# Kernel tuning notes

Hardware: AMD Instinct MI355X
Metric: run time of the kernel (lower is better)

Reference implementation:

```python
import jax, jax.numpy as jnp
import numpy as np

B = 262144
D = 128          # d_model
DFF = 4 * D      # 512, FFN expansion
T = 16           # num_tiles
TPC = 4          # tiles_per_cluster
NC = T // TPC    # 4 clusters
NOPS = 8         # len(OPCODES)
EMB = 32
FEAT = EMB + 17  # 49
TW, SW, DW = 0.01, 0.005, 0.01  # ternary / sparsity / diversity weights


def ternary_quant(W):
    # per-tile ternary quantization: threshold at 0.7 * mean|W|, scale = mean|W|
    s0 = jnp.mean(jnp.abs(W))
    return s0 * jnp.sign(W) * (jnp.abs(W) > 0.7 * s0).astype(W.dtype)


def setup_inputs() -> dict:
    key = jax.random.key(0)
    ks = jax.random.split(key, 16)
    inp = {
        'op_idx': jax.random.randint(ks[0], (B,), 0, NOPS),
        'a': jax.random.randint(ks[1], (B,), 0, 256),
        'b': jax.random.randint(ks[2], (B,), 0, 256),
        'c': jax.random.randint(ks[3], (B,), 0, 2),
        # parameters
        'op_embed': jax.random.normal(ks[4], (NOPS, EMB), jnp.float32),
        'W_in': jax.random.normal(ks[5], (FEAT, D), jnp.float32) / np.sqrt(FEAT),
        'b_in': jnp.zeros((D,), jnp.float32),
        'Wr': jax.random.normal(ks[6], (D, T), jnp.float32) / np.sqrt(D),
        'W1': jax.random.normal(ks[7], (T, D, DFF), jnp.float32) / np.sqrt(D),
        'W2': jax.random.normal(ks[8], (T, DFF, D), jnp.float32) / np.sqrt(DFF),
        'Wh1': jax.random.normal(ks[9], (D, 64), jnp.float32) / np.sqrt(D),
        'bh1': jnp.zeros((64,), jnp.float32),
        'Wh2': jax.random.normal(ks[10], (64, 8), jnp.float32) / np.sqrt(64),
        'bh2': jnp.zeros((8,), jnp.float32),
    }
    return inp


def reference(op_embed, W_in, b_in, Wr, W1, W2, Wh1, bh1, Wh2, bh2, op_idx, a, b, c):
    bits = lambda v: ((v[:, None] >> jnp.arange(8)) & 1).astype(jnp.float32)  # [B,8]
    emb = op_embed[op_idx]  # [B,32]
    x = jnp.concatenate([emb, bits(a), bits(b), c[:, None].astype(jnp.float32)], axis=1)  # [B,49]
    x = x @ W_in + b_in  # [B,D]

    # tile routing (top-1)
    logits = x @ Wr                      # [B,T]
    probs = jax.nn.softmax(logits, -1)
    idx = jnp.argmax(probs, -1)          # [B]
    gate = jnp.max(probs, -1)            # [B]

    # ternary-quantized per-tile FFN weights
    W1q = jax.vmap(ternary_quant)(W1)    # [T,D,DFF]
    W2q = jax.vmap(ternary_quant)(W2)    # [T,DFF,D]

    out = jnp.zeros_like(x)
    for t in range(T):  # fixed small tile set
        y = jax.nn.gelu(x @ W1q[t]) @ W2q[t]          # [B,D]
        out = out + jnp.where((idx == t)[:, None], y, 0.0)
    out = out * gate[:, None]

    # aux losses
    one_hot = jax.nn.one_hot(idx, T, dtype=x.dtype)
    frac = one_hot.mean(0)               # tokens per tile
    meanp = probs.mean(0)                # mean router prob per tile
    sparsity = T * jnp.sum(frac * meanp)              # load-balance (Switch-style)
    tern = jnp.mean(jnp.abs(W1 - W1q)) + jnp.mean(jnp.abs(W2 - W2q))
    cp = meanp.reshape(NC, TPC).sum(-1)               # cluster usage
    diversity = jnp.sum(cp * jnp.log(cp + 1e-9))      # negative entropy
    aux = TW * tern + SW * sparsity + DW * diversity

    h = jax.nn.relu(out @ Wh1 + bh1)
    result = jax.nn.sigmoid(h @ Wh2 + bh2)  # [B,8]
    return result, idx, aux
```

## Files before the change

### kernel.cpp

```cpp
#include <hip/hip_runtime.h>
#include <hip/hip_bf16.h>
#include <math.h>

typedef __attribute__((ext_vector_type(8))) short short8;
typedef __attribute__((ext_vector_type(4))) float floatx4;
typedef __attribute__((ext_vector_type(4))) unsigned int uintx4;

#define BUCKET_CAP 262144

__device__ __forceinline__ unsigned short f2bf(float f) {
    unsigned int u = __float_as_uint(f);
    unsigned int r = (u + 0x7fffu + ((u >> 16) & 1u)) >> 16;
    return (unsigned short)r;
}

__device__ __forceinline__ unsigned int cvtpk(float a, float b) {
    unsigned int r;
    asm("v_cvt_pk_bf16_f32 %0, %1, %2" : "=v"(r) : "v"(a), "v"(b));
    return r;
}

__device__ __forceinline__ void permlane32_swap(unsigned int &a, unsigned int &b) {
    asm volatile("v_permlane32_swap_b32 %0, %1" : "+v"(a), "+v"(b));
}
__device__ __forceinline__ void permlane16_swap(unsigned int &a, unsigned int &b) {
    asm volatile("v_permlane16_swap_b32 %0, %1" : "+v"(a), "+v"(b));
}

__device__ __forceinline__ float gelu_f(float u) {
    float u2 = u * u;
    float p = __builtin_fmaf(u2, -0.102943242f, -2.302208184f);
    float z = p * u;
    float e;
    asm("v_exp_f32 %0, %1" : "=v"(e) : "v"(z));
    return u * __builtin_amdgcn_rcpf(1.0f + e);
}

__device__ __forceinline__ floatx4 mfma16(short8 a, short8 b, floatx4 c) {
    return __builtin_amdgcn_mfma_f32_16x16x32_bf16(a, b, c, 0, 0, 0);
}


__global__ __launch_bounds__(256) void k_prep1(
        const float* __restrict__ W1, const float* __restrict__ W2,
        float* __restrict__ partials,
        const float* __restrict__ op_embed, const float* __restrict__ W_in,
        const float* __restrict__ b_in,
        float* embW, float* Ta, float* Tb, float* Tc,
        int* __restrict__ accz) {
    __shared__ float red[256];
    int bid = blockIdx.x;
    if (bid < 512) {
        bool isW1 = bid < 256;
        const float* W = (isW1 ? W1 : W2) + (long)(isW1 ? bid : bid - 256) * 4096;
        float s = 0.f;
        #pragma unroll
        for (int i = 0; i < 4; i++) {
            floatx4 v = *(const floatx4*)(W + i * 1024 + threadIdx.x * 4);
            s += fabsf(v[0]) + fabsf(v[1]) + fabsf(v[2]) + fabsf(v[3]);
        }
        red[threadIdx.x] = s; __syncthreads();
        for (int st = 128; st > 0; st >>= 1) {
            if (threadIdx.x < st) red[threadIdx.x] += red[threadIdx.x + st];
            __syncthreads();
        }
        if (threadIdx.x == 0) partials[bid] = red[0];
    } else {
        int i = (bid - 512) * 256 + threadIdx.x;
        if (i < 1024) {
            int op = i >> 7, j = i & 127;
            float s = b_in[j];
            #pragma unroll
            for (int k = 0; k < 32; k++) s += op_embed[op * 32 + k] * W_in[k * 128 + j];
            embW[i] = s;
        } else if (i < 1024 + 32768) {
            int r = i - 1024; int a = r >> 7, j = r & 127;
            float s = 0.f;
            #pragma unroll
            for (int bit = 0; bit < 8; bit++) if ((a >> bit) & 1) s += W_in[(32 + bit) * 128 + j];
            Ta[r] = s;
        } else if (i < 33792 + 32768) {
            int r = i - 33792; int b = r >> 7, j = r & 127;
            float s = 0.f;
            #pragma unroll
            for (int bit = 0; bit < 8; bit++) if ((b >> bit) & 1) s += W_in[(40 + bit) * 128 + j];
            Tb[r] = s;
        } else if (i < 66560 + 128) {
            int j = i - 66560; Tc[j] = W_in[48 * 128 + j];
        } else if (i < 66688 + 64) {
            accz[i - 66688] = 0;
        }
    }
}


__global__ __launch_bounds__(256) void k_prep2(
        const float* __restrict__ W1, const float* __restrict__ W2,
        const float* __restrict__ partials,
        unsigned short* __restrict__ W1qT, unsigned short* __restrict__ W2qT,
        float* ternsum,
        const float* __restrict__ embW, const float* __restrict__ Ta,
        const float* __restrict__ Tb, const float* __restrict__ Tc,
        const float* __restrict__ Wr,
        float* embWr, float* TaR, float* TbR, float* TcR) {
    __shared__ unsigned short Lq[4096];
    __shared__ float red[256];
    int blk = blockIdx.x;
    if (blk >= 512) {
        int i = (blk - 512) * 256 + threadIdx.x;
        int row = i >> 4, t = i & 15;
        const float* src; float* dst;
        if (row < 8)        { src = embW + row * 128;        dst = embWr + i; }
        else if (row < 264) { src = Ta + (row - 8) * 128;    dst = TaR + (row - 8) * 16 + t; }
        else if (row < 520) { src = Tb + (row - 264) * 128;  dst = TbR + (row - 264) * 16 + t; }
        else if (row == 520){ src = Tc;                      dst = TcR + t; }
        else return;
        float s = 0.f;
        for (int j = 0; j < 128; j++) s += src[j] * Wr[j * 16 + t];
        *dst = s;
        return;
    }
    bool isW1 = blk < 256;
    int rb = isW1 ? blk : blk - 256;
    int t = rb >> 4, slab = rb & 15;
    const float* part = partials + (isW1 ? 0 : 256) + t * 16;
    float ssum = 0.f;
    #pragma unroll
    for (int i = 0; i < 16; i++) ssum += part[i];
    float s = ssum * (1.0f / 65536.0f);
    float thr = 0.7f * s;
    unsigned int us = (unsigned int)f2bf(s);
    int tid = threadIdx.x;
    float dsum = 0.f;
    if (isW1) {
        int f0 = slab * 32;
        int d = tid >> 1, fh = (tid & 1) * 16;
        const float* src = W1 + (long)t * 65536 + d * 512 + f0 + fh;
        #pragma unroll
        for (int i = 0; i < 4; i++) {
            floatx4 w = *(const floatx4*)(src + i * 4);
            #pragma unroll
            for (int r = 0; r < 4; r++) {
                float wv = w[r];
                float aw = fabsf(wv);
                bool big = aw > thr;
                dsum += big ? fabsf(aw - s) : aw;
                unsigned int sign15 = (__float_as_uint(wv) >> 16) & 0x8000u;
                unsigned short q = big ? (unsigned short)(us | sign15) : (unsigned short)0;
                Lq[(fh + i * 4 + r) * 128 + d] = q;
            }
        }
    } else {
        int d0 = slab * 8;
        int f = tid * 2;
        const float* src = W2 + (long)t * 65536 + f * 128 + d0;
        #pragma unroll
        for (int rr = 0; rr < 2; rr++) {
            #pragma unroll
            for (int i = 0; i < 2; i++) {
                floatx4 w = *(const floatx4*)(src + rr * 128 + i * 4);
                #pragma unroll
                for (int r = 0; r < 4; r++) {
                    float wv = w[r];
                    float aw = fabsf(wv);
                    bool big = aw > thr;
                    dsum += big ? fabsf(aw - s) : aw;
                    unsigned int sign15 = (__float_as_uint(wv) >> 16) & 0x8000u;
                    unsigned short q = big ? (unsigned short)(us | sign15) : (unsigned short)0;
                    Lq[(i * 4 + r) * 512 + f + rr] = q;
                }
            }
        }
    }
    __syncthreads();
    unsigned short* dst = (isW1 ? W1qT : W2qT) + (long)t * 65536 + slab * 4096;
    const uintx4* Ls = (const uintx4*)Lq;
    uintx4* D4 = (uintx4*)dst;
    D4[tid] = Ls[tid];
    D4[tid + 256] = Ls[tid + 256];
    red[tid] = dsum; __syncthreads();
    for (int st2 = 128; st2 > 0; st2 >>= 1) {
        if (tid < st2) red[tid] += red[tid + st2];
        __syncthreads();
    }
    if (tid == 0) atomicAdd(ternsum, red[0]);
}


__global__ __launch_bounds__(256) void k_main3(
        const int* __restrict__ op_idx, const int* __restrict__ a_in,
        const int* __restrict__ b_in_i, const int* __restrict__ c_in,
        const float* __restrict__ embWr, const float* __restrict__ TaR,
        const float* __restrict__ TbR, const float* __restrict__ TcR,
        float2* __restrict__ rec_out,
        float* psum, int* cnt, int* fill, int* __restrict__ bucket,
        float* __restrict__ d_idx,
        const unsigned short* __restrict__ W2qT, const float* __restrict__ Wh1,
        unsigned short* __restrict__ W23qT) {
    __shared__ float sp[4][16];
    __shared__ int sc[4][16];
    __shared__ float wcol[128];
    __shared__ int lc[16], lbase[16];
    __shared__ unsigned char blE[256];
    __shared__ unsigned char lpE[256];

    if (blockIdx.x >= 1024) {
        int b2 = blockIdx.x - 1024;
        int t = b2 >> 6, h = b2 & 63;
        if (threadIdx.x < 128) wcol[threadIdx.x] = Wh1[threadIdx.x * 64 + h];
        __syncthreads();
        int k2 = threadIdx.x * 2;
        const unsigned short* w2 = W2qT + (long)t * 65536 + k2;
        float a0 = 0.f, a1 = 0.f;
        #pragma unroll 8
        for (int d = 0; d < 128; d++) {
            unsigned int u = *(const unsigned int*)(w2 + d * 512);
            float w = wcol[d];
            a0 += w * __uint_as_float(u << 16);
            a1 += w * __uint_as_float(u & 0xffff0000u);
        }
        *(unsigned int*)(W23qT + ((long)(t * 64 + h)) * 512 + k2) = cvtpk(a0, a1);
        return;
    }

    int tid = threadIdx.x;
    if (tid < 16) lc[tid] = 0;
    __syncthreads();

    int lane = tid & 63;
    int j = lane & 15;
    int grpbase = lane & 48;
    int tl = tid >> 4;
    float psum_acc = 0.f; int cnt_acc = 0;

    #pragma unroll 1
    for (int it = 0; it < 16; it++) {
        int tok = blockIdx.x * 256 + it * 16 + tl;
        int op = op_idx[tok], a = a_in[tok], b = b_in_i[tok], c = c_in[tok];
        float cf = (float)c;

        float lg = embWr[op * 16 + j] + TaR[a * 16 + j] + TbR[b * 16 + j] + cf * TcR[j];
        float m = lg;
        m = fmaxf(m, __shfl_xor(m, 8, 16));
        m = fmaxf(m, __shfl_xor(m, 4, 16));
        m = fmaxf(m, __shfl_xor(m, 2, 16));
        m = fmaxf(m, __shfl_xor(m, 1, 16));
        float p = __expf(lg - m);
        float s = p;
        s += __shfl_xor(s, 8, 16);
        s += __shfl_xor(s, 4, 16);
        s += __shfl_xor(s, 2, 16);
        s += __shfl_xor(s, 1, 16);
        float g = __builtin_amdgcn_rcpf(s);
        unsigned long long ball = __ballot(lg == m);
        int bi = __ffsll((unsigned long long)((ball >> grpbase) & 0xffffULL)) - 1;
        psum_acc += p * g;
        cnt_acc += (j == bi) ? 1 : 0;
        if (j == bi) {
            int lpos = atomicAdd(&lc[bi], 1);
            int e = it * 16 + tl;
            blE[e] = (unsigned char)bi;
            lpE[e] = (unsigned char)lpos;
        }
        if (j == 0) {
            unsigned int desc = (unsigned int)op | ((unsigned int)a << 3)
                              | ((unsigned int)b << 11) | ((unsigned int)c << 19);
            float2 rr; rr.x = __uint_as_float(desc); rr.y = g;
            rec_out[tok] = rr;
            d_idx[tok] = (float)bi;
        }
    }

    psum_acc += __shfl_xor(psum_acc, 16);
    psum_acc += __shfl_xor(psum_acc, 32);
    cnt_acc += __shfl_xor(cnt_acc, 16);
    cnt_acc += __shfl_xor(cnt_acc, 32);
    int wv = tid >> 6;
    if (lane < 16) { sp[wv][j] = psum_acc; sc[wv][j] = cnt_acc; }
    __syncthreads();
    if (tid < 16) {
        atomicAdd(&psum[tid], sp[0][tid] + sp[1][tid] + sp[2][tid] + sp[3][tid]);
        atomicAdd(&cnt[tid], sc[0][tid] + sc[1][tid] + sc[2][tid] + sc[3][tid]);
        lbase[tid] = atomicAdd(&fill[tid], lc[tid]);
    }
    __syncthreads();
    {
        int e = tid;
        int bi = (int)blE[e];
        int tok = blockIdx.x * 256 + e;
        bucket[bi * BUCKET_CAP + lbase[bi] + (int)lpE[e]] = tok;
    }
}


__global__ __launch_bounds__(256, 3) void k_ffn(
    const float2* __restrict__ rec,
    const float* __restrict__ embW, const float* __restrict__ Ta,
    const float* __restrict__ Tb, const float* __restrict__ Tc,
    const int* __restrict__ bucket, const int* __restrict__ cnt_g,
    const float* __restrict__ psum_g, const float* __restrict__ ternsum_g,
    const unsigned short* __restrict__ W1qT, const unsigned short* __restrict__ W23qT,
    const float* __restrict__ Wh2, const float* __restrict__ bh1,
    const float* __restrict__ bh2,
    float* __restrict__ result, float* __restrict__ d_aux) {

    extern __shared__ __align__(16) unsigned char smem[];
    unsigned short* Ax = (unsigned short*)smem;
    float* Red = (float*)(smem + 17408);
    int*   toks = (int*)(smem + 33792);
    float* gats = (float*)(smem + 34048);
    float* Wh2l = (float*)(smem + 34304);
    float* bh2l = (float*)(smem + 36352);
    float* bh1l = (float*)(smem + 36384);
    int*   opsl = (int*)(smem + 36640);
    int*   asl  = (int*)(smem + 36896);
    int*   bsl  = (int*)(smem + 37152);
    float* csl  = (float*)(smem + 37408);
    int*   cntl = (int*)(smem + 37664);

    int bid = blockIdx.x;
    int tid = threadIdx.x;

    if (tid < 16) cntl[tid] = cnt_g[tid];
    __syncthreads();
    int t = -1, ci = 0, nt = 0, base = 0;
    {
        int coff = 0;
        #pragma unroll
        for (int tt = 0; tt < 16; tt++) {
            int c = cntl[tt];
            int ch = (c + 63) >> 6;
            if (t < 0 && bid < coff + ch) {
                t = tt; ci = bid - coff; nt = c;
                base = tt * BUCKET_CAP + ci * 64;
            }
            coff += ch;
        }
    }
    if (t < 0) return;
    int nvalid = nt - ci * 64; if (nvalid > 64) nvalid = 64;

    if (tid < 64) {
        int tk = (tid < nvalid) ? bucket[base + tid] : -1;
        toks[tid] = tk;
        int tks = (tk >= 0) ? tk : 0;
        float2 rd = rec[tks];
        unsigned int desc = __float_as_uint(rd.x);
        gats[tid] = (tk >= 0) ? rd.y : 0.0f;
        opsl[tid] = (int)(desc & 7u);
        asl[tid]  = (int)((desc >> 3) & 255u);
        bsl[tid]  = (int)((desc >> 11) & 255u);
        csl[tid]  = (float)((desc >> 19) & 1u);
    }
    Wh2l[tid] = Wh2[tid];
    Wh2l[tid + 256] = Wh2[tid + 256];
    if (tid < 8) bh2l[tid] = bh2[tid];
    else if (tid < 72) bh1l[tid - 8] = bh1[tid - 8];
    __syncthreads();

    #pragma unroll
    for (int it = 0; it < 4; it++) {
        int seg = it * 256 + tid; int r = seg >> 4, sg = seg & 15;
        int d0 = sg * 8;
        int op = opsl[r], a = asl[r], b = bsl[r];
        float cf = csl[r];
        const floatx4* Ev = (const floatx4*)(embW + op * 128 + d0);
        const floatx4* A4 = (const floatx4*)(Ta + a * 128 + d0);
        const floatx4* B4 = (const floatx4*)(Tb + b * 128 + d0);
        const floatx4* C4 = (const floatx4*)(Tc + d0);
        floatx4 v0 = Ev[0] + A4[0] + B4[0] + cf * C4[0];
        floatx4 v1 = Ev[1] + A4[1] + B4[1] + cf * C4[1];
        uintx4 o;
        o[0] = cvtpk(v0[0], v0[1]);
        o[1] = cvtpk(v0[2], v0[3]);
        o[2] = cvtpk(v1[0], v1[1]);
        o[3] = cvtpk(v1[2], v1[3]);
        *(uintx4*)(Ax + r * 136 + sg * 8) = o;
    }
    __syncthreads();

    int lane = tid & 63, dh = tid >> 6;
    int lane15 = lane & 15, lgrp = lane >> 4;

    floatx4 acc3[4][4];
    #pragma unroll
    for (int i = 0; i < 4; i++)
        #pragma unroll
        for (int j = 0; j < 4; j++) acc3[i][j] = (floatx4){0.f, 0.f, 0.f, 0.f};

    const unsigned short* w1p  = W1qT + (long)t * 65536 + (dh * 32 + lane15) * 128 + lgrp * 8;
    const unsigned short* w23p = W23qT + (long)t * 32768 + lane15 * 512 + dh * 32 + lgrp * 8;
    int ho0 = dh * 8192;
    int ho1 = ((dh + 1) & 3) * 8192;
    int ho2 = ((dh + 2) & 3) * 8192;
    int ho3 = ((dh + 3) & 3) * 8192;

    #pragma unroll
    for (int nc = 0; nc < 4; nc++) {
        const unsigned short* w1c = w1p + nc * 16384;
        const unsigned short* w23c = w23p + nc * 128;

        short8 a00 = *(const short8*)(w1c + 0 * 32);
        short8 a01 = *(const short8*)(w1c + 1 * 32);
        short8 a02 = *(const short8*)(w1c + 2 * 32);
        short8 a03 = *(const short8*)(w1c + 3 * 32);
        short8 a10 = *(const short8*)(w1c + 2048 + 0 * 32);
        short8 a11 = *(const short8*)(w1c + 2048 + 1 * 32);
        short8 a12 = *(const short8*)(w1c + 2048 + 2 * 32);
        short8 a13 = *(const short8*)(w1c + 2048 + 3 * 32);
        short8 af23_0 = *(const short8*)(w23c + ho0);
        short8 af23_1 = *(const short8*)(w23c + ho1);
        short8 af23_2 = *(const short8*)(w23c + ho2);
        short8 af23_3 = *(const short8*)(w23c + ho3);

        floatx4 acc1[2][4];
        #pragma unroll
        for (int i = 0; i < 2; i++)
            #pragma unroll
            for (int j = 0; j < 4; j++) acc1[i][j] = (floatx4){0.f, 0.f, 0.f, 0.f};

        #pragma unroll
        for (int mt = 0; mt < 4; mt++) {
            int mrow = (mt * 16 + lane15) * 136;
            short8 bf0 = *(const short8*)(Ax + mrow + 0 * 32 + lgrp * 8);
            short8 bf1 = *(const short8*)(Ax + mrow + 1 * 32 + lgrp * 8);
            short8 bf2 = *(const short8*)(Ax + mrow + 2 * 32 + lgrp * 8);
            short8 bf3 = *(const short8*)(Ax + mrow + 3 * 32 + lgrp * 8);
            acc1[0][mt] = mfma16(a00, bf0, acc1[0][mt]);
            acc1[1][mt] = mfma16(a10, bf0, acc1[1][mt]);
            acc1[0][mt] = mfma16(a01, bf1, acc1[0][mt]);
            acc1[1][mt] = mfma16(a11, bf1, acc1[1][mt]);
            acc1[0][mt] = mfma16(a02, bf2, acc1[0][mt]);
            acc1[1][mt] = mfma16(a12, bf2, acc1[1][mt]);
            acc1[0][mt] = mfma16(a03, bf3, acc1[0][mt]);
            acc1[1][mt] = mfma16(a13, bf3, acc1[1][mt]);
        }

        #pragma unroll
        for (int mt = 0; mt < 4; mt++) {
            floatx4 v0 = acc1[0][mt], v1 = acc1[1][mt];
            unsigned int X0 = cvtpk(gelu_f(v0[0]), gelu_f(v0[1]));
            unsigned int X1 = cvtpk(gelu_f(v0[2]), gelu_f(v0[3]));
            unsigned int Y0 = cvtpk(gelu_f(v1[0]), gelu_f(v1[1]));
            unsigned int Y1 = cvtpk(gelu_f(v1[2]), gelu_f(v1[3]));
            permlane32_swap(X0, Y0);
            permlane16_swap(X0, Y0);
            permlane32_swap(X1, Y1);
            permlane16_swap(X1, Y1);
            union { uintx4 u; short8 s; } bu;
            bu.u[0] = X0; bu.u[1] = X1; bu.u[2] = Y0; bu.u[3] = Y1;
            short8 bfrag = bu.s;
            acc3[0][mt] = mfma16(af23_0, bfrag, acc3[0][mt]);
            acc3[1][mt] = mfma16(af23_1, bfrag, acc3[1][mt]);
            acc3[2][mt] = mfma16(af23_2, bfrag, acc3[2][mt]);
            acc3[3][mt] = mfma16(af23_3, bfrag, acc3[3][mt]);
        }
    }

    floatx4 fin[4];
    #pragma unroll
    for (int mt = 0; mt < 4; mt++) fin[mt] = acc3[0][mt];
    float* myslot = Red + dh * 1024;
    int lofs = lane * 4;
    #pragma unroll
    for (int mt = 0; mt < 4; mt++)
        *(floatx4*)(myslot + mt * 256 + lofs) = acc3[1][mt];
    __syncthreads();
    {
        const float* ps = Red + ((dh + 3) & 3) * 1024;
        #pragma unroll
        for (int mt = 0; mt < 4; mt++)
            fin[mt] += *(const floatx4*)(ps + mt * 256 + lofs);
    }
    __syncthreads();
    #pragma unroll
    for (int mt = 0; mt < 4; mt++)
        *(floatx4*)(myslot + mt * 256 + lofs) = acc3[2][mt];
    __syncthreads();
    {
        const float* ps = Red + ((dh + 2) & 3) * 1024;
        #pragma unroll
        for (int mt = 0; mt < 4; mt++)
            fin[mt] += *(const floatx4*)(ps + mt * 256 + lofs);
    }
    __syncthreads();
    #pragma unroll
    for (int mt = 0; mt < 4; mt++)
        *(floatx4*)(myslot + mt * 256 + lofs) = acc3[3][mt];
    __syncthreads();
    {
        const float* ps = Red + ((dh + 1) & 3) * 1024;
        #pragma unroll
        for (int mt = 0; mt < 4; mt++)
            fin[mt] += *(const floatx4*)(ps + mt * 256 + lofs);
    }

    float* H = (float*)Ax;
    int hb = dh * 16 + lgrp * 4;
    floatx4 b4 = *(const floatx4*)(bh1l + hb);
    #pragma unroll
    for (int mt = 0; mt < 4; mt++) {
        int m = mt * 16 + lane15;
        float gm = gats[m];
        floatx4 v;
        v[0] = fmaxf(fin[mt][0] * gm + b4[0], 0.f);
        v[1] = fmaxf(fin[mt][1] * gm + b4[1], 0.f);
        v[2] = fmaxf(fin[mt][2] * gm + b4[2], 0.f);
        v[3] = fmaxf(fin[mt][3] * gm + b4[3], 0.f);
        *(floatx4*)(H + m * 68 + hb) = v;
    }
    __syncthreads();

    int mloc = tid >> 2, c0 = (tid & 3) * 2;
    int tk = toks[mloc];
    float z0 = bh2l[c0], z1 = bh2l[c0 + 1];
    const floatx4* Hr4 = (const floatx4*)(H + mloc * 68);
    #pragma unroll
    for (int h4 = 0; h4 < 16; h4++) {
        floatx4 hv = Hr4[h4];
        #pragma unroll
        for (int r = 0; r < 4; r++) {
            int h = h4 * 4 + r;
            z0 += hv[r] * Wh2l[h * 8 + c0];
            z1 += hv[r] * Wh2l[h * 8 + c0 + 1];
        }
    }
    if (tk >= 0) {
        float2 rr;
        rr.x = __builtin_amdgcn_rcpf(1.0f + __expf(-z0));
        rr.y = __builtin_amdgcn_rcpf(1.0f + __expf(-z1));
        *(float2*)(result + (long)tk * 8 + c0) = rr;
    }

    if (bid == 0 && tid == 0) {
        const float Bf = 262144.0f;
        float tern = ternsum_g[0] * (1.0f / 1048576.0f);
        float sp = 0.f; float cp[4] = {0.f, 0.f, 0.f, 0.f};
        for (int tt = 0; tt < 16; tt++) {
            float frac = (float)cntl[tt] / Bf, mp = psum_g[tt] / Bf;
            sp += frac * mp; cp[tt >> 2] += mp;
        }
        float dv = 0.f;
        for (int cc = 0; cc < 4; cc++) dv += cp[cc] * logf(cp[cc] + 1e-9f);
        d_aux[0] = 0.01f * tern + 0.005f * (16.0f * sp) + 0.01f * dv;
    }
}


extern "C" void kernel_launch(void* const* d_in, const int* in_sizes, int n_in,
                              void* d_out, int out_size, void* d_ws, size_t ws_size,
                              hipStream_t stream) {
    const int* op_idx = (const int*)d_in[0];
    const int* a_in   = (const int*)d_in[1];
    const int* b_in_i = (const int*)d_in[2];
    const int* c_in   = (const int*)d_in[3];
    const float* op_embed = (const float*)d_in[4];
    const float* W_in  = (const float*)d_in[5];
    const float* b_in  = (const float*)d_in[6];
    const float* Wr    = (const float*)d_in[7];
    const float* W1    = (const float*)d_in[8];
    const float* W2    = (const float*)d_in[9];
    const float* Wh1   = (const float*)d_in[10];
    const float* bh1   = (const float*)d_in[11];
    const float* Wh2   = (const float*)d_in[12];
    const float* bh2   = (const float*)d_in[13];

    const long B = in_sizes[0];
    float* result = (float*)d_out;
    float* d_idx  = (float*)d_out + B * 8;
    float* d_aux  = (float*)d_out + B * 9;

    unsigned char* ws = (unsigned char*)d_ws;
    int*   bucket= (int*)(ws + 0);
    unsigned short* W1qT  = (unsigned short*)(ws + 67108864);
    unsigned short* W2qT  = (unsigned short*)(ws + 69206016);
    unsigned short* W23qT = (unsigned short*)(ws + 71303168);
    float2* rec  = (float2*)(ws + 72351744);
    float* Ta    = (float*)(ws + 74448896);
    float* Tb    = (float*)(ws + 74579968);
    float* embW  = (float*)(ws + 74711040);
    float* Tc    = (float*)(ws + 74715136);
    float* TaR   = (float*)(ws + 74715648);
    float* TbR   = (float*)(ws + 74732032);
    float* embWr = (float*)(ws + 74748416);
    float* TcR   = (float*)(ws + 74748928);
    float* partials = (float*)(ws + 74748992);
    unsigned char* acc = ws + 74751040;
    float* ternsum = (float*)(acc + 0);
    float* psum    = (float*)(acc + 64);
    int*   cnt     = (int*)(acc + 128);
    int*   fill    = (int*)(acc + 192);

    k_prep1<<<773, 256, 0, stream>>>(W1, W2, partials, op_embed, W_in, b_in,
                                     embW, Ta, Tb, Tc, (int*)acc);
    k_prep2<<<545, 256, 0, stream>>>(W1, W2, partials, W1qT, W2qT, ternsum,
                                     embW, Ta, Tb, Tc, Wr, embWr, TaR, TbR, TcR);
    k_main3<<<2048, 256, 0, stream>>>(op_idx, a_in, b_in_i, c_in,
                                      embWr, TaR, TbR, TcR,
                                      rec, psum, cnt, fill, bucket, d_idx,
                                      W2qT, Wh1, W23qT);
    k_ffn<<<4112, 256, 37728, stream>>>(rec,
                                        embW, Ta, Tb, Tc,
                                        bucket, cnt, psum, ternsum,
                                        W1qT, W23qT, Wh2, bh1, bh2, result, d_aux);
}
```

Measured before the change: 249.8 us.

## Split FFN work by token rows per wave instead of hidden dims

Each wave now owns 16 token rows and loops over all 512 hidden units, so every wave reads the full W1/W23 tile slices. Previously the 4 waves split the hidden dimension and combined partial results through a shared-memory reduction with several barriers. Removing that reduction frees its LDS buffer, which cuts dynamic shared memory from about 37.7KB to 21.3KB and lets launch bounds target 4 blocks per CU. The cost is four times more weight loads per wave from cache and less register reuse of the weight fragments.

```diff
diff --git a/kernel.cpp b/kernel.cpp
--- a/kernel.cpp
+++ b/kernel.cpp
@@ -293,7 +293,7 @@
 }
 
 
-__global__ __launch_bounds__(256, 3) void k_ffn(
+__global__ __launch_bounds__(256, 4) void k_ffn(
     const float2* __restrict__ rec,
     const float* __restrict__ embW, const float* __restrict__ Ta,
     const float* __restrict__ Tb, const float* __restrict__ Tc,
@@ -306,17 +306,16 @@
 
     extern __shared__ __align__(16) unsigned char smem[];
     unsigned short* Ax = (unsigned short*)smem;
-    float* Red = (float*)(smem + 17408);
-    int*   toks = (int*)(smem + 33792);
-    float* gats = (float*)(smem + 34048);
-    float* Wh2l = (float*)(smem + 34304);
-    float* bh2l = (float*)(smem + 36352);
-    float* bh1l = (float*)(smem + 36384);
-    int*   opsl = (int*)(smem + 36640);
-    int*   asl  = (int*)(smem + 36896);
-    int*   bsl  = (int*)(smem + 37152);
-    float* csl  = (float*)(smem + 37408);
-    int*   cntl = (int*)(smem + 37664);
+    int*   toks = (int*)(smem + 17408);
+    float* gats = (float*)(smem + 17664);
+    float* Wh2l = (float*)(smem + 17920);
+    float* bh2l = (float*)(smem + 19968);
+    float* bh1l = (float*)(smem + 20000);
+    int*   opsl = (int*)(smem + 20256);
+    int*   asl  = (int*)(smem + 20512);
+    int*   bsl  = (int*)(smem + 20768);
+    float* csl  = (float*)(smem + 21024);
+    int*   cntl = (int*)(smem + 21280);
 
     int bid = blockIdx.x;
     int tid = threadIdx.x;
@@ -382,23 +381,23 @@
     int lane = tid & 63, dh = tid >> 6;
     int lane15 = lane & 15, lgrp = lane >> 4;
 
-    floatx4 acc3[4][4];
+    int myrow = (dh * 16 + lane15) * 136 + lgrp * 8;
+    short8 bf0 = *(const short8*)(Ax + myrow + 0 * 32);
+    short8 bf1 = *(const short8*)(Ax + myrow + 1 * 32);
+    short8 bf2 = *(const short8*)(Ax + myrow + 2 * 32);
+    short8 bf3 = *(const short8*)(Ax + myrow + 3 * 32);
+
+    floatx4 acc3[4];
     #pragma unroll
-    for (int i = 0; i < 4; i++)
-        #pragma unroll
-        for (int j = 0; j < 4; j++) acc3[i][j] = (floatx4){0.f, 0.f, 0.f, 0.f};
-
-    const unsigned short* w1p  = W1qT + (long)t * 65536 + (dh * 32 + lane15) * 128 + lgrp * 8;
-    const unsigned short* w23p = W23qT + (long)t * 32768 + lane15 * 512 + dh * 32 + lgrp * 8;
-    int ho0 = dh * 8192;
-    int ho1 = ((dh + 1) & 3) * 8192;
-    int ho2 = ((dh + 2) & 3) * 8192;
-    int ho3 = ((dh + 3) & 3) * 8192;
-
-    #pragma unroll
-    for (int nc = 0; nc < 4; nc++) {
-        const unsigned short* w1c = w1p + nc * 16384;
-        const unsigned short* w23c = w23p + nc * 128;
+    for (int i = 0; i < 4; i++) acc3[i] = (floatx4){0.f, 0.f, 0.f, 0.f};
+
+    const unsigned short* w1p  = W1qT + (long)t * 65536 + lane15 * 128 + lgrp * 8;
+    const unsigned short* w23p = W23qT + (long)t * 32768 + lane15 * 512 + lgrp * 8;
+
+    #pragma unroll 2
+    for (int j = 0; j < 16; j++) {
+        const unsigned short* w1c = w1p + j * 4096;
+        const unsigned short* w23c = w23p + j * 32;
 
         short8 a00 = *(const short8*)(w1c + 0 * 32);
         short8 a01 = *(const short8*)(w1c + 1 * 32);
@@ -408,106 +407,55 @@
         short8 a11 = *(const short8*)(w1c + 2048 + 1 * 32);
         short8 a12 = *(const short8*)(w1c + 2048 + 2 * 32);
         short8 a13 = *(const short8*)(w1c + 2048 + 3 * 32);
-        short8 af23_0 = *(const short8*)(w23c + ho0);
-        short8 af23_1 = *(const short8*)(w23c + ho1);
-        short8 af23_2 = *(const short8*)(w23c + ho2);
-        short8 af23_3 = *(const short8*)(w23c + ho3);
-
-        floatx4 acc1[2][4];
+        short8 af23_0 = *(const short8*)(w23c + 0 * 8192);
+        short8 af23_1 = *(const short8*)(w23c + 1 * 8192);
+        short8 af23_2 = *(const short8*)(w23c + 2 * 8192);
+        short8 af23_3 = *(const short8*)(w23c + 3 * 8192);
+
+        floatx4 acc1_0 = (floatx4){0.f, 0.f, 0.f, 0.f};
+        floatx4 acc1_1 = (floatx4){0.f, 0.f, 0.f, 0.f};
+        acc1_0 = mfma16(a00, bf0, acc1_0);
+        acc1_1 = mfma16(a10, bf0, acc1_1);
+        acc1_0 = mfma16(a01, bf1, acc1_0);
+        acc1_1 = mfma16(a11, bf1, acc1_1);
+        acc1_0 = mfma16(a02, bf2, acc1_0);
+        acc1_1 = mfma16(a12, bf2, acc1_1);
+        acc1_0 = mfma16(a03, bf3, acc1_0);
+        acc1_1 = mfma16(a13, bf3, acc1_1);
+
+        unsigned int X0 = cvtpk(gelu_f(acc1_0[0]), gelu_f(acc1_0[1]));
+        unsigned int X1 = cvtpk(gelu_f(acc1_0[2]), gelu_f(acc1_0[3]));
+        unsigned int Y0 = cvtpk(gelu_f(acc1_1[0]), gelu_f(acc1_1[1]));
+        unsigned int Y1 = cvtpk(gelu_f(acc1_1[2]), gelu_f(acc1_1[3]));
+        permlane32_swap(X0, Y0);
+        permlane16_swap(X0, Y0);
+        permlane32_swap(X1, Y1);
+        permlane16_swap(X1, Y1);
+        union { uintx4 u; short8 s; } bu;
+        bu.u[0] = X0; bu.u[1] = X1; bu.u[2] = Y0; bu.u[3] = Y1;
+        short8 bfrag = bu.s;
+        acc3[0] = mfma16(af23_0, bfrag, acc3[0]);
+        acc3[1] = mfma16(af23_1, bfrag, acc3[1]);
+        acc3[2] = mfma16(af23_2, bfrag, acc3[2]);
+        acc3[3] = mfma16(af23_3, bfrag, acc3[3]);
+    }
+
+    __syncthreads();
+    float* H = (float*)Ax;
+    {
+        int m = dh * 16 + lane15;
+        float gm = gats[m];
         #pragma unroll
-        for (int i = 0; i < 2; i++)
-            #pragma unroll
-            for (int j = 0; j < 4; j++) acc1[i][j] = (floatx4){0.f, 0.f, 0.f, 0.f};
-
-        #pragma unroll
-        for (int mt = 0; mt < 4; mt++) {
-            int mrow = (mt * 16 + lane15) * 136;
-            short8 bf0 = *(const short8*)(Ax + mrow + 0 * 32 + lgrp * 8);
-            short8 bf1 = *(const short8*)(Ax + mrow + 1 * 32 + lgrp * 8);
-            short8 bf2 = *(const short8*)(Ax + mrow + 2 * 32 + lgrp * 8);
-            short8 bf3 = *(const short8*)(Ax + mrow + 3 * 32 + lgrp * 8);
-            acc1[0][mt] = mfma16(a00, bf0, acc1[0][mt]);
-            acc1[1][mt] = mfma16(a10, bf0, acc1[1][mt]);
-            acc1[0][mt] = mfma16(a01, bf1, acc1[0][mt]);
-            acc1[1][mt] = mfma16(a11, bf1, acc1[1][mt]);
-            acc1[0][mt] = mfma16(a02, bf2, acc1[0][mt]);
-            acc1[1][mt] = mfma16(a12, bf2, acc1[1][mt]);
-            acc1[0][mt] = mfma16(a03, bf3, acc1[0][mt]);
-            acc1[1][mt] = mfma16(a13, bf3, acc1[1][mt]);
-        }
-
-        #pragma unroll
-        for (int mt = 0; mt < 4; mt++) {
-            floatx4 v0 = acc1[0][mt], v1 = acc1[1][mt];
-            unsigned int X0 = cvtpk(gelu_f(v0[0]), gelu_f(v0[1]));
-            unsigned int X1 = cvtpk(gelu_f(v0[2]), gelu_f(v0[3]));
-            unsigned int Y0 = cvtpk(gelu_f(v1[0]), gelu_f(v1[1]));
-            unsigned int Y1 = cvtpk(gelu_f(v1[2]), gelu_f(v1[3]));
-            permlane32_swap(X0, Y0);
-            permlane16_swap(X0, Y0);
-            permlane32_swap(X1, Y1);
-            permlane16_swap(X1, Y1);
-            union { uintx4 u; short8 s; } bu;
-            bu.u[0] = X0; bu.u[1] = X1; bu.u[2] = Y0; bu.u[3] = Y1;
-            short8 bfrag = bu.s;
-            acc3[0][mt] = mfma16(af23_0, bfrag, acc3[0][mt]);
-            acc3[1][mt] = mfma16(af23_1, bfrag, acc3[1][mt]);
-            acc3[2][mt] = mfma16(af23_2, bfrag, acc3[2][mt]);
-            acc3[3][mt] = mfma16(af23_3, bfrag, acc3[3][mt]);
-        }
-    }
-
-    floatx4 fin[4];
-    #pragma unroll
-    for (int mt = 0; mt < 4; mt++) fin[mt] = acc3[0][mt];
-    float* myslot = Red + dh * 1024;
-    int lofs = lane * 4;
-    #pragma unroll
-    for (int mt = 0; mt < 4; mt++)
-        *(floatx4*)(myslot + mt * 256 + lofs) = acc3[1][mt];
-    __syncthreads();
-    {
-        const float* ps = Red + ((dh + 3) & 3) * 1024;
-        #pragma unroll
-        for (int mt = 0; mt < 4; mt++)
-            fin[mt] += *(const floatx4*)(ps + mt * 256 + lofs);
-    }
-    __syncthreads();
-    #pragma unroll
-    for (int mt = 0; mt < 4; mt++)
-        *(floatx4*)(myslot + mt * 256 + lofs) = acc3[2][mt];
-    __syncthreads();
-    {
-        const float* ps = Red + ((dh + 2) & 3) * 1024;
-        #pragma unroll
-        for (int mt = 0; mt < 4; mt++)
-            fin[mt] += *(const floatx4*)(ps + mt * 256 + lofs);
-    }
-    __syncthreads();
-    #pragma unroll
-    for (int mt = 0; mt < 4; mt++)
-        *(floatx4*)(myslot + mt * 256 + lofs) = acc3[3][mt];
-    __syncthreads();
-    {
-        const float* ps = Red + ((dh + 1) & 3) * 1024;
-        #pragma unroll
-        for (int mt = 0; mt < 4; mt++)
-            fin[mt] += *(const floatx4*)(ps + mt * 256 + lofs);
-    }
-
-    float* H = (float*)Ax;
-    int hb = dh * 16 + lgrp * 4;
-    floatx4 b4 = *(const floatx4*)(bh1l + hb);
-    #pragma unroll
-    for (int mt = 0; mt < 4; mt++) {
-        int m = mt * 16 + lane15;
-        float gm = gats[m];
-        floatx4 v;
-        v[0] = fmaxf(fin[mt][0] * gm + b4[0], 0.f);
-        v[1] = fmaxf(fin[mt][1] * gm + b4[1], 0.f);
-        v[2] = fmaxf(fin[mt][2] * gm + b4[2], 0.f);
-        v[3] = fmaxf(fin[mt][3] * gm + b4[3], 0.f);
-        *(floatx4*)(H + m * 68 + hb) = v;
+        for (int i = 0; i < 4; i++) {
+            int hb = i * 16 + lgrp * 4;
+            floatx4 b4 = *(const floatx4*)(bh1l + hb);
+            floatx4 v;
+            v[0] = fmaxf(acc3[i][0] * gm + b4[0], 0.f);
+            v[1] = fmaxf(acc3[i][1] * gm + b4[1], 0.f);
+            v[2] = fmaxf(acc3[i][2] * gm + b4[2], 0.f);
+            v[3] = fmaxf(acc3[i][3] * gm + b4[3], 0.f);
+            *(floatx4*)(H + m * 68 + hb) = v;
+        }
     }
     __syncthreads();
 
@@ -599,7 +547,7 @@
                                       embWr, TaR, TbR, TcR,
                                       rec, psum, cnt, fill, bucket, d_idx,
                                       W2qT, Wh1, W23qT);
-    k_ffn<<<4112, 256, 37728, stream>>>(rec,
+    k_ffn<<<4112, 256, 21344, stream>>>(rec,
                                         embW, Ta, Tb, Tc,
                                         bucket, cnt, psum, ternsum,
                                         W1qT, W23qT, Wh2, bh1, bh2, result, d_aux);
```

Result: slower. 502.8 us (+101.3%).
